# Optimization experiments

Measured on AMD Instinct MI355X. Metric: run time of the kernel, lower is better.

The kernel has to match this reference:

```python
import jax, jax.numpy as jnp
import numpy as np

N, DIN = 8192, 768
DH1, DO1 = 64, 64
DH2, DO2 = 32, 64


def setup_inputs() -> dict:
    key = jax.random.key(0)
    ks = jax.random.split(key, 12)
    s = lambda *sh: 0.02
    inp = {
        "X": jax.random.normal(ks[0], (N, DIN), jnp.float32),
        "A": jax.random.randint(ks[1], (N, N), 0, 2, jnp.int32),
        # GAT layer 1: W (din->dh), a (2dh), W2 (dh->dout) + bias
        "W1": jax.random.normal(ks[2], (DIN, DH1), jnp.float32) * 0.02,
        "a1": jax.random.normal(ks[3], (2 * DH1,), jnp.float32) * 0.02,
        "W21": jax.random.normal(ks[4], (DH1, DO1), jnp.float32) * 0.02,
        "b21": jnp.zeros((DO1,), jnp.float32),
        # GAT layer 2
        "Wg2": jax.random.normal(ks[5], (DO1, DH2), jnp.float32) * 0.02,
        "a2": jax.random.normal(ks[6], (2 * DH2,), jnp.float32) * 0.02,
        "W22": jax.random.normal(ks[7], (DH2, DO2), jnp.float32) * 0.02,
        "b22": jnp.zeros((DO2,), jnp.float32),
        # MLP head: 64 -> 64 -> 2
        "M1": jax.random.normal(ks[8], (DO2, 64), jnp.float32) * 0.02,
        "bm1": jnp.zeros((64,), jnp.float32),
        "M2": jax.random.normal(ks[9], (64, 2), jnp.float32) * 0.02,
        "bm2": jnp.zeros((2,), jnp.float32),
    }
    return inp


def _tiny_gat(X, A, W, a, W2, b2):
    # H = X @ W; e_ij = a . [H_i, H_j] = H_i@a_src + H_j@a_dst (same math,
    # no N x N x 2dh intermediate)
    H = X @ W                      # [N, dh]
    dh = W.shape[1]
    e = (H @ a[:dh])[:, None] + (H @ a[dh:])[None, :]   # [N, N]
    e = jnp.where(A == 0, jnp.float32(-1e9), e)
    alpha = jax.nn.softmax(e, axis=1)                   # softmax over neighbors j
    Z = alpha @ H                                       # [N, dh]
    return jax.nn.elu(Z @ W2 + b2)


def reference(X, A, W1, a1, W21, b21, Wg2, a2, W22, b22, M1, bm1, M2, bm2):
    Z = _tiny_gat(X, A, W1, a1, W21, b21)    # [N, 64]
    Z = _tiny_gat(Z, A, Wg2, a2, W22, b22)   # [N, 64]
    g = Z.mean(axis=0)                       # [64]
    h = jax.nn.relu(g @ M1 + bm1)
    return h @ M2 + bm2                      # [2]
```

## Files before the change

kernel.cpp:

```cpp
#include <hip/hip_runtime.h>


#define NN 8192

typedef __attribute__((ext_vector_type(8))) short s16x8;
typedef __attribute__((ext_vector_type(4))) float f32x4;
union V16 { uint4 u; s16x8 s; };

static constexpr size_t OFF_WBITS = 0;
static constexpr size_t OFF_GT1H  = (size_t)8 << 20;
static constexpr size_t OFF_GT1L  = (size_t)9 << 20;
static constexpr size_t OFF_U1    = (size_t)10 << 20;
static constexpr size_t OFF_DEN1  = ((size_t)10 << 20) + 32 * 1024;
static constexpr size_t OFF_GT2H  = ((size_t)10 << 20) + 128 * 1024;
static constexpr size_t OFF_GT2L  = ((size_t)10 << 20) + 896 * 1024;
static constexpr size_t OFF_GPART = ((size_t)11 << 20) + 768 * 1024;
static constexpr size_t OFF_NUMP  = (size_t)12 << 20;

__device__ __forceinline__ float elu_f(float x) {
    return x > 0.f ? x : expm1f(x);
}
__device__ __forceinline__ unsigned int bf16_rne(float x) {
    unsigned int u = __float_as_uint(x);
    return (u + 0x7FFFu + ((u >> 16) & 1u)) >> 16;
}
__device__ __forceinline__ unsigned int split_pack(float g) {
    unsigned int hi = bf16_rne(g);
    float fhi = __uint_as_float(hi << 16);
    unsigned int lo = bf16_rne(g - fhi);
    return (hi << 16) | lo;
}

__global__ __launch_bounds__(512) void k_xw1(const float* __restrict__ X,
                                             const float* __restrict__ W1,
                                             const float* __restrict__ a1,
                                             unsigned int* __restrict__ Gt1h,
                                             unsigned int* __restrict__ Gt1l,
                                             float* __restrict__ u1) {
    __shared__ float Xt[32][65];
    __shared__ float red[32][17];
    __shared__ float us[32];
    __shared__ unsigned int Gsh[64][33];
    const int tid = threadIdx.x;
    const int row = tid & 31, cg = tid >> 5;
    const int row0 = blockIdx.x * 32;
    float acc[4];
#pragma unroll
    for (int i = 0; i < 4; ++i) acc[i] = 0.f;
    const float4* X4 = (const float4*)X;
    for (int k0 = 0; k0 < 768; k0 += 64) {
        __syncthreads();
        {
            int r = tid >> 4, q = tid & 15;
            float4 v = X4[(size_t)(row0 + r) * 192 + (k0 >> 2) + q];
            Xt[r][q * 4 + 0] = v.x; Xt[r][q * 4 + 1] = v.y;
            Xt[r][q * 4 + 2] = v.z; Xt[r][q * 4 + 3] = v.w;
        }
        __syncthreads();
        const float4* W4 = (const float4*)(W1 + (size_t)k0 * 64);
        for (int kk = 0; kk < 64; ++kk) {
            float x = Xt[row][kk];
            float4 w = W4[kk * 16 + cg];
            acc[0] += x * w.x; acc[1] += x * w.y;
            acc[2] += x * w.z; acc[3] += x * w.w;
        }
    }
    float p = 0.f;
#pragma unroll
    for (int i = 0; i < 4; ++i) p += acc[i] * a1[64 + cg * 4 + i];
    red[row][cg] = p;
    __syncthreads();
    if (tid < 32) {
        float d = 0.f;
#pragma unroll
        for (int g = 0; g < 16; ++g) d += red[tid][g];
        float uv = expf(d);
        u1[row0 + tid] = uv;
        us[tid] = uv;
    }
    __syncthreads();
    float uv = us[row];
#pragma unroll
    for (int i = 0; i < 4; ++i)
        Gsh[cg * 4 + i][row] = split_pack(acc[i] * uv);
    __syncthreads();
    if (tid < 256) {
        const int mt = tid >> 6, lane = tid & 63;
        const int feat = mt * 16 + (lane & 15), quad = lane >> 4;
        uint4 hv, lv;
        unsigned int g0, g1;
#define PACK_Q(Q, FX)                                            \
        g0 = Gsh[feat][quad * 8 + 2 * Q];                        \
        g1 = Gsh[feat][quad * 8 + 2 * Q + 1];                    \
        hv.FX = (g0 >> 16) | (g1 & 0xFFFF0000u);                 \
        lv.FX = (g0 & 0xFFFFu) | (g1 << 16);
        PACK_Q(0, x) PACK_Q(1, y) PACK_Q(2, z) PACK_Q(3, w)
#undef PACK_Q
        size_t base = ((size_t)(mt * 256 + blockIdx.x) * 64 + lane) * 4;
        *(uint4*)(Gt1h + base) = hv;
        *(uint4*)(Gt1l + base) = lv;
    }
}

__global__ __launch_bounds__(256) void k_pack(const int* __restrict__ A,
                                              const float* __restrict__ u1,
                                              unsigned int* __restrict__ Wb32,
                                              float* __restrict__ den1) {
    __shared__ unsigned short msh[8][512];
    const int tid = threadIdx.x, wv = tid >> 6, lane = tid & 63;
    const int row0 = blockIdx.x * 8;
    float dsum0 = 0.f, dsum1 = 0.f;
    const int r0 = row0 + wv * 2, r1 = r0 + 1;
    for (int c = 0; c < 8; ++c) {
        const int j = c * 1024 + lane * 16;
        const int4* A0 = (const int4*)(A + (size_t)r0 * NN + j);
        const int4* A1 = (const int4*)(A + (size_t)r1 * NN + j);
        const float4* U4 = (const float4*)(u1 + j);
        int4 a0 = A0[0], a1 = A0[1], a2 = A0[2], a3 = A0[3];
        int4 b0 = A1[0], b1 = A1[1], b2 = A1[2], b3 = A1[3];
        float4 u0 = U4[0], u4 = U4[1], u8 = U4[2], uc = U4[3];
        unsigned int m0 = 0, m1 = 0;
#define DO4(AV, BV, UV, SH)                                            \
        m0 |= ((AV.x != 0) << (SH)) | ((AV.y != 0) << (SH + 1)) |      \
              ((AV.z != 0) << (SH + 2)) | ((AV.w != 0) << (SH + 3));   \
        m1 |= ((BV.x != 0) << (SH)) | ((BV.y != 0) << (SH + 1)) |      \
              ((BV.z != 0) << (SH + 2)) | ((BV.w != 0) << (SH + 3));   \
        dsum0 += (AV.x != 0 ? UV.x : 0.f) + (AV.y != 0 ? UV.y : 0.f) + \
                 (AV.z != 0 ? UV.z : 0.f) + (AV.w != 0 ? UV.w : 0.f);  \
        dsum1 += (BV.x != 0 ? UV.x : 0.f) + (BV.y != 0 ? UV.y : 0.f) + \
                 (BV.z != 0 ? UV.z : 0.f) + (BV.w != 0 ? UV.w : 0.f);
        DO4(a0, b0, u0, 0) DO4(a1, b1, u4, 4) DO4(a2, b2, u8, 8) DO4(a3, b3, uc, 12)
#undef DO4
        msh[wv * 2 + 0][c * 64 + lane] = (unsigned short)m0;
        msh[wv * 2 + 1][c * 64 + lane] = (unsigned short)m1;
    }
#pragma unroll
    for (int off = 32; off; off >>= 1) {
        dsum0 += __shfl_down(dsum0, off);
        dsum1 += __shfl_down(dsum1, off);
    }
    if (lane == 0) { den1[r0] = dsum0; den1[r1] = dsum1; }
    __syncthreads();
    {
        const int r = tid >> 5, i = tid & 31;
        const uint4* src = (const uint4*)&msh[r][0];
        uint4* dst = (uint4*)(Wb32 + (size_t)(row0 + r) * 256);
        dst[i] = src[i];
        dst[i + 32] = src[i + 32];
    }
}

__device__ __forceinline__ void build_lut(uint4* lut, int tid) {
    unsigned int b = (unsigned int)(tid & 255);
    uint4 e;
    e.x = ((b & 1u)   ? 0x3F80u : 0u) | ((b & 2u)   ? 0x3F800000u : 0u);
    e.y = ((b & 4u)   ? 0x3F80u : 0u) | ((b & 8u)   ? 0x3F800000u : 0u);
    e.z = ((b & 16u)  ? 0x3F80u : 0u) | ((b & 32u)  ? 0x3F800000u : 0u);
    e.w = ((b & 64u)  ? 0x3F80u : 0u) | ((b & 128u) ? 0x3F800000u : 0u);
    if (tid < 256) lut[tid] = e;
}

__global__ __launch_bounds__(256) void k_attn1(const unsigned int* __restrict__ Wb32,
                                               const unsigned int* __restrict__ Gt1h,
                                               const unsigned int* __restrict__ Gt1l,
                                               float* __restrict__ num1p) {
    __shared__ uint4 lut[256];
    __shared__ unsigned int bw[64 * 20];
    const int tid = threadIdx.x, wv = tid >> 6, lane = tid & 63;
    const int node0 = blockIdx.x * 64;
    const int kt0 = blockIdx.y * 16;
    build_lut(lut, tid);
    {
        const int r = tid >> 2, part = tid & 3;
        const uint4* src = (const uint4*)(Wb32 + (size_t)(node0 + r) * 256 + kt0 + part * 4);
        *(uint4*)&bw[r * 20 + part * 4] = src[0];
    }
    __syncthreads();
    const int n = lane & 15, quad = lane >> 4;
    const int brow = (wv * 16 + n) * 20;
    f32x4 acc[4];
#pragma unroll
    for (int mt = 0; mt < 4; ++mt) acc[mt] = (f32x4){0.f, 0.f, 0.f, 0.f};
#pragma unroll 2
    for (int ks = 0; ks < 16; ++ks) {
        unsigned int bits = bw[brow + ks];
        unsigned int byt = (bits >> (quad * 8)) & 0xFFu;
        V16 bf; bf.u = lut[byt];
#pragma unroll
        for (int mt = 0; mt < 4; ++mt) {
            size_t base = ((size_t)(mt * 256 + kt0 + ks) * 64 + lane) * 4;
            V16 ah, al;
            ah.u = *(const uint4*)(Gt1h + base);
            al.u = *(const uint4*)(Gt1l + base);
            acc[mt] = __builtin_amdgcn_mfma_f32_16x16x32_bf16(ah.s, bf.s, acc[mt], 0, 0, 0);
            acc[mt] = __builtin_amdgcn_mfma_f32_16x16x32_bf16(al.s, bf.s, acc[mt], 0, 0, 0);
        }
    }
    const int node = node0 + wv * 16 + n;
    const int s = blockIdx.y;
#pragma unroll
    for (int mt = 0; mt < 4; ++mt)
        *(f32x4*)&num1p[((size_t)s * NN + node) * 64 + mt * 16 + quad * 4] = acc[mt];
}

__global__ __launch_bounds__(512) void k_ep1(const float* __restrict__ num1p,
                                             const float* __restrict__ den1,
                                             const float* __restrict__ W21,
                                             const float* __restrict__ b21,
                                             const float* __restrict__ Wg2,
                                             const float* __restrict__ a2,
                                             unsigned int* __restrict__ Gt2h,
                                             unsigned int* __restrict__ Gt2l) {
    __shared__ float w21sh[64 * 64];
    __shared__ float wg2sh[64 * 32];
    __shared__ float zsh[8][64];
    __shared__ float osh[8][64];
    __shared__ unsigned int g2sh[32][33];
    __shared__ unsigned int u2sh[32];
    const int tid = threadIdx.x, wv = tid >> 6, lane = tid & 63;
    const int node0 = blockIdx.x * 32;
    {
        const float4* s4 = (const float4*)W21;
        float4* d4 = (float4*)w21sh;
        d4[tid] = s4[tid];
        d4[tid + 512] = s4[tid + 512];
        ((float4*)wg2sh)[tid] = ((const float4*)Wg2)[tid];
    }
    const float bb = b21[lane];
    const int l32 = lane & 31;
    const float a2v = (lane < 32) ? a2[32 + l32] : 0.f;
    __syncthreads();
    for (int it = 0; it < 4; ++it) {
        const int node = node0 + wv * 4 + it;
        float sacc = 0.f;
#pragma unroll
        for (int sp = 0; sp < 16; ++sp)
            sacc += num1p[((size_t)sp * NN + node) * 64 + lane];
        zsh[wv][lane] = sacc / den1[node];
        __builtin_amdgcn_wave_barrier();
        float o0 = 0.f, o1 = 0.f, o2 = 0.f, o3 = 0.f;
        for (int c = 0; c < 64; c += 4) {
            o0 += zsh[wv][c + 0] * w21sh[(c + 0) * 64 + lane];
            o1 += zsh[wv][c + 1] * w21sh[(c + 1) * 64 + lane];
            o2 += zsh[wv][c + 2] * w21sh[(c + 2) * 64 + lane];
            o3 += zsh[wv][c + 3] * w21sh[(c + 3) * 64 + lane];
        }
        float o = elu_f(bb + ((o0 + o1) + (o2 + o3)));
        osh[wv][lane] = o;
        __builtin_amdgcn_wave_barrier();
        float h0 = 0.f, h1 = 0.f;
        for (int c = 0; c < 64; c += 2) {
            h0 += osh[wv][c + 0] * wg2sh[(c + 0) * 32 + l32];
            h1 += osh[wv][c + 1] * wg2sh[(c + 1) * 32 + l32];
        }
        float hval = h0 + h1;
        float pp = hval * a2v;
#pragma unroll
        for (int off = 32; off; off >>= 1) pp += __shfl_down(pp, off);
        float d2 = __shfl(pp, 0);
        float uu = expf(d2);
        const int nodeloc = wv * 4 + it;
        if (lane == 0) u2sh[nodeloc] = split_pack(uu);
        if (lane < 32) g2sh[l32][nodeloc] = split_pack(uu * hval);
    }
    __syncthreads();
    if (tid < 192) {
        const int mt = tid >> 6, lane2 = tid & 63;
        const int ml = lane2 & 15, quad = lane2 >> 4;
        uint4 hv, lv;
        unsigned int g0, g1;
#define PACK_Q(Q, F)                                                   \
        {                                                              \
            int j0 = quad * 8 + 2 * Q;                                 \
            if (mt < 2) { g0 = g2sh[mt * 16 + ml][j0];                 \
                          g1 = g2sh[mt * 16 + ml][j0 + 1]; }           \
            else if (ml == 0) { g0 = u2sh[j0]; g1 = u2sh[j0 + 1]; }    \
            else { g0 = 0; g1 = 0; }                                   \
            hv.F = (g0 >> 16) | (g1 & 0xFFFF0000u);                    \
            lv.F = (g0 & 0xFFFFu) | (g1 << 16);                        \
        }
        PACK_Q(0, x) PACK_Q(1, y) PACK_Q(2, z) PACK_Q(3, w)
#undef PACK_Q
        size_t base = ((size_t)(mt * 256 + blockIdx.x) * 64 + lane2) * 4;
        *(uint4*)(Gt2h + base) = hv;
        *(uint4*)(Gt2l + base) = lv;
    }
}

__global__ __launch_bounds__(256) void k_attn2(const unsigned int* __restrict__ Wb32,
                                               const unsigned int* __restrict__ Gt2h,
                                               const unsigned int* __restrict__ Gt2l,
                                               float* __restrict__ num2p) {
    __shared__ uint4 lut[256];
    __shared__ unsigned int bw[64 * 20];
    const int tid = threadIdx.x, wv = tid >> 6, lane = tid & 63;
    const int node0 = blockIdx.x * 64;
    const int kt0 = blockIdx.y * 16;
    build_lut(lut, tid);
    {
        const int r = tid >> 2, part = tid & 3;
        const uint4* src = (const uint4*)(Wb32 + (size_t)(node0 + r) * 256 + kt0 + part * 4);
        *(uint4*)&bw[r * 20 + part * 4] = src[0];
    }
    __syncthreads();
    const int n = lane & 15, quad = lane >> 4;
    const int brow = (wv * 16 + n) * 20;
    f32x4 acc[3];
#pragma unroll
    for (int mt = 0; mt < 3; ++mt) acc[mt] = (f32x4){0.f, 0.f, 0.f, 0.f};
#pragma unroll 2
    for (int ks = 0; ks < 16; ++ks) {
        unsigned int bits = bw[brow + ks];
        unsigned int byt = (bits >> (quad * 8)) & 0xFFu;
        V16 bf; bf.u = lut[byt];
#pragma unroll
        for (int mt = 0; mt < 3; ++mt) {
            size_t base = ((size_t)(mt * 256 + kt0 + ks) * 64 + lane) * 4;
            V16 ah, al;
            ah.u = *(const uint4*)(Gt2h + base);
            al.u = *(const uint4*)(Gt2l + base);
            acc[mt] = __builtin_amdgcn_mfma_f32_16x16x32_bf16(ah.s, bf.s, acc[mt], 0, 0, 0);
            acc[mt] = __builtin_amdgcn_mfma_f32_16x16x32_bf16(al.s, bf.s, acc[mt], 0, 0, 0);
        }
    }
    const int node = node0 + wv * 16 + n;
    const int s = blockIdx.y;
#pragma unroll
    for (int mt = 0; mt < 3; ++mt)
        *(f32x4*)&num2p[((size_t)s * NN + node) * 48 + mt * 16 + quad * 4] = acc[mt];
}

__global__ __launch_bounds__(512) void k_ep2(const float* __restrict__ num2p,
                                             const float* __restrict__ W22,
                                             const float* __restrict__ b22,
                                             float* __restrict__ gpart) {
    __shared__ float w22sh[32 * 64];
    __shared__ float zsh[8][32];
    __shared__ float gsh[8][64];
    const int tid = threadIdx.x, wv = tid >> 6, lane = tid & 63;
    ((float4*)w22sh)[tid] = ((const float4*)W22)[tid];
    const float bb = b22[lane];
    __syncthreads();
    const int row = blockIdx.x * 8 + wv;
    float val = 0.f;
    if (lane < 33) {
#pragma unroll
        for (int sp = 0; sp < 16; ++sp)
            val += num2p[((size_t)sp * NN + row) * 48 + lane];
    }
    float den = __shfl(val, 32);
    if (lane < 32) zsh[wv][lane] = val / den;
    __builtin_amdgcn_wave_barrier();
    float o0 = 0.f, o1 = 0.f;
    for (int c = 0; c < 32; c += 2) {
        o0 += zsh[wv][c + 0] * w22sh[(c + 0) * 64 + lane];
        o1 += zsh[wv][c + 1] * w22sh[(c + 1) * 64 + lane];
    }
    gsh[wv][lane] = elu_f(bb + o0 + o1);
    __syncthreads();
    if (tid < 64) {
        float s = 0.f;
#pragma unroll
        for (int w = 0; w < 8; ++w) s += gsh[w][tid];
        gpart[(size_t)blockIdx.x * 64 + tid] = s;
    }
}

__global__ __launch_bounds__(256) void k_head(const float* __restrict__ gpart,
                                              const float* __restrict__ M1,
                                              const float* __restrict__ bm1,
                                              const float* __restrict__ M2,
                                              const float* __restrict__ bm2,
                                              float* __restrict__ outp) {
    __shared__ float part[4][64];
    __shared__ float gsh[64];
    __shared__ float hsh[64];
    const int tid = threadIdx.x, col = tid & 63, p = tid >> 6;
    float s = 0.f;
    for (int b = p * 256; b < p * 256 + 256; ++b)
        s += gpart[(size_t)b * 64 + col];
    part[p][col] = s;
    __syncthreads();
    if (tid < 64)
        gsh[tid] = (part[0][tid] + part[1][tid] + part[2][tid] + part[3][tid])
                   * (1.0f / 8192.0f);
    __syncthreads();
    if (tid < 64) {
        float h = bm1[tid];
        for (int c = 0; c < 64; ++c) h += gsh[c] * M1[c * 64 + tid];
        hsh[tid] = h > 0.f ? h : 0.f;
    }
    __syncthreads();
    if (tid < 2) {
        float o = bm2[tid];
        for (int j = 0; j < 64; ++j) o += hsh[j] * M2[j * 2 + tid];
        outp[tid] = o;
    }
}

extern "C" void kernel_launch(void* const* d_in, const int* in_sizes, int n_in,
                              void* d_out, int out_size, void* d_ws, size_t ws_size,
                              hipStream_t stream) {
    const float* X   = (const float*)d_in[0];
    const int*   A   = (const int*)  d_in[1];
    const float* W1  = (const float*)d_in[2];
    const float* a1  = (const float*)d_in[3];
    const float* W21 = (const float*)d_in[4];
    const float* b21 = (const float*)d_in[5];
    const float* Wg2 = (const float*)d_in[6];
    const float* a2  = (const float*)d_in[7];
    const float* W22 = (const float*)d_in[8];
    const float* b22 = (const float*)d_in[9];
    const float* M1  = (const float*)d_in[10];
    const float* bm1 = (const float*)d_in[11];
    const float* M2  = (const float*)d_in[12];
    const float* bm2 = (const float*)d_in[13];
    float* out = (float*)d_out;

    char* ws = (char*)d_ws;
    unsigned int* Wbits = (unsigned int*)(ws + OFF_WBITS);
    unsigned int* Gt1h  = (unsigned int*)(ws + OFF_GT1H);
    unsigned int* Gt1l  = (unsigned int*)(ws + OFF_GT1L);
    unsigned int* Gt2h  = (unsigned int*)(ws + OFF_GT2H);
    unsigned int* Gt2l  = (unsigned int*)(ws + OFF_GT2L);
    float* u1    = (float*)(ws + OFF_U1);
    float* den1  = (float*)(ws + OFF_DEN1);
    float* gpart = (float*)(ws + OFF_GPART);
    float* nump  = (float*)(ws + OFF_NUMP);

    k_xw1  <<<256, 512, 0, stream>>>(X, W1, a1, Gt1h, Gt1l, u1);
    k_pack <<<1024, 256, 0, stream>>>(A, u1, Wbits, den1);
    k_attn1<<<dim3(128, 16), 256, 0, stream>>>(Wbits, Gt1h, Gt1l, nump);
    k_ep1  <<<256, 512, 0, stream>>>(nump, den1, W21, b21, Wg2, a2, Gt2h, Gt2l);
    k_attn2<<<dim3(128, 16), 256, 0, stream>>>(Wbits, Gt2h, Gt2l, nump);
    k_ep2  <<<1024, 512, 0, stream>>>(nump, W22, b22, gpart);
    k_head <<<1, 256, 0, stream>>>(gpart, M1, bm1, M2, bm2, out);
}
```

Before: 591.1 us.

## Move X@W1 to split-bf16 MFMA and restructure attention waves by feature tile

The scalar FP32 X@W1 GEMM is replaced by a split-K MFMA kernel. X is split three ways and W1 two ways into bf16 pieces to keep near-fp32 accuracy, W1 is pre-packed by a setup kernel, and a combine kernel reduces the partials, computes u1 and packs Gt1. The attention kernels now give each wave one feature tile and loop over four node tiles. This loads each G fragment once per wave instead of per feature tile, and the shared-memory LUT is replaced by arithmetic bit-to-bf16 expansion. It adds extra launches and a partial-sum buffer, and in attn2 one wave idles.

```diff
diff --git a/kernel.cpp b/kernel.cpp
--- a/kernel.cpp
+++ b/kernel.cpp
@@ -16,6 +16,9 @@
 static constexpr size_t OFF_GT2L  = ((size_t)10 << 20) + 896 * 1024;
 static constexpr size_t OFF_GPART = ((size_t)11 << 20) + 768 * 1024;
 static constexpr size_t OFF_NUMP  = (size_t)12 << 20;
+static constexpr size_t OFF_WTAH  = (size_t)44 << 20;
+static constexpr size_t OFF_WTAL  = ((size_t)44 << 20) + 128 * 1024;
+static constexpr size_t OFF_DP    = (size_t)45 << 20;
 
 __device__ __forceinline__ float elu_f(float x) {
     return x > 0.f ? x : expm1f(x);
@@ -30,70 +33,144 @@
     unsigned int lo = bf16_rne(g - fhi);
     return (hi << 16) | lo;
 }
-
-__global__ __launch_bounds__(512) void k_xw1(const float* __restrict__ X,
-                                             const float* __restrict__ W1,
-                                             const float* __restrict__ a1,
-                                             unsigned int* __restrict__ Gt1h,
-                                             unsigned int* __restrict__ Gt1l,
-                                             float* __restrict__ u1) {
-    __shared__ float Xt[32][65];
-    __shared__ float red[32][17];
+__device__ __forceinline__ void split3(float f, unsigned int& h, unsigned int& m,
+                                       unsigned int& l) {
+    h = bf16_rne(f);
+    float fh = __uint_as_float(h << 16);
+    float r1 = f - fh;
+    m = bf16_rne(r1);
+    float fm = __uint_as_float(m << 16);
+    l = bf16_rne(r1 - fm);
+}
+__device__ __forceinline__ unsigned int bits2bf(unsigned int b2) {
+    return (b2 & 1u) * 0x3F80u + (b2 & 2u) * 0x1FC00000u;
+}
+
+__global__ __launch_bounds__(256) void k_wsetup(const float* __restrict__ W1,
+                                                unsigned int* __restrict__ WtAh,
+                                                unsigned int* __restrict__ WtAl) {
+    const int t = blockIdx.x * 256 + threadIdx.x;
+    const int tile = t >> 6, lane = t & 63;
+    const int mt = tile / 24, kt = tile % 24;
+    const int feat = mt * 16 + (lane & 15), quad = lane >> 4;
+    uint4 hv, lv;
+    unsigned int h0, l0, h1, l1;
+#define WQ(Q, F)                                                        \
+    {                                                                   \
+        int k0 = kt * 32 + quad * 8 + 2 * Q;                            \
+        float w0 = W1[(size_t)k0 * 64 + feat];                          \
+        float w1 = W1[(size_t)(k0 + 1) * 64 + feat];                    \
+        h0 = bf16_rne(w0); l0 = bf16_rne(w0 - __uint_as_float(h0 << 16));\
+        h1 = bf16_rne(w1); l1 = bf16_rne(w1 - __uint_as_float(h1 << 16));\
+        hv.F = h0 | (h1 << 16);                                         \
+        lv.F = l0 | (l1 << 16);                                         \
+    }
+    WQ(0, x) WQ(1, y) WQ(2, z) WQ(3, w)
+#undef WQ
+    size_t base = (size_t)((mt * 24 + kt) * 64 + lane) * 4;
+    *(uint4*)(WtAh + base) = hv;
+    *(uint4*)(WtAl + base) = lv;
+}
+
+__global__ __launch_bounds__(256) void k_xw1m(const float* __restrict__ X,
+                                              const unsigned int* __restrict__ WtAh,
+                                              const unsigned int* __restrict__ WtAl,
+                                              float* __restrict__ Dp) {
+    const int tid = threadIdx.x, wv = tid >> 6, lane = tid & 63;
+    const int n = lane & 15, quad = lane >> 4;
+    const int node = blockIdx.x * 64 + wv * 16 + n;
+    const int ntg = blockIdx.x * 4 + wv;
+    const int ks = blockIdx.y;
+    f32x4 acc[4];
+#pragma unroll
+    for (int mt = 0; mt < 4; ++mt) acc[mt] = (f32x4){0.f, 0.f, 0.f, 0.f};
+    const float4* X4 = (const float4*)X;
+    for (int kk = 0; kk < 6; ++kk) {
+        const int kt = ks * 6 + kk;
+        float4 x01 = X4[(size_t)node * 192 + kt * 8 + quad * 2];
+        float4 x23 = X4[(size_t)node * 192 + kt * 8 + quad * 2 + 1];
+        float xf[8] = {x01.x, x01.y, x01.z, x01.w, x23.x, x23.y, x23.z, x23.w};
+        V16 bh, bm, bl;
+        unsigned int* bhp = (unsigned int*)&bh.u;
+        unsigned int* bmp = (unsigned int*)&bm.u;
+        unsigned int* blp = (unsigned int*)&bl.u;
+#pragma unroll
+        for (int q = 0; q < 4; ++q) {
+            unsigned int h0, m0, l0, h1, m1, l1;
+            split3(xf[2 * q], h0, m0, l0);
+            split3(xf[2 * q + 1], h1, m1, l1);
+            bhp[q] = h0 | (h1 << 16);
+            bmp[q] = m0 | (m1 << 16);
+            blp[q] = l0 | (l1 << 16);
+        }
+#pragma unroll
+        for (int mt = 0; mt < 4; ++mt) {
+            size_t base = (size_t)((mt * 24 + kt) * 64 + lane) * 4;
+            V16 awh, awl;
+            awh.u = *(const uint4*)(WtAh + base);
+            awl.u = *(const uint4*)(WtAl + base);
+            acc[mt] = __builtin_amdgcn_mfma_f32_16x16x32_bf16(awh.s, bh.s, acc[mt], 0, 0, 0);
+            acc[mt] = __builtin_amdgcn_mfma_f32_16x16x32_bf16(awh.s, bm.s, acc[mt], 0, 0, 0);
+            acc[mt] = __builtin_amdgcn_mfma_f32_16x16x32_bf16(awh.s, bl.s, acc[mt], 0, 0, 0);
+            acc[mt] = __builtin_amdgcn_mfma_f32_16x16x32_bf16(awl.s, bh.s, acc[mt], 0, 0, 0);
+            acc[mt] = __builtin_amdgcn_mfma_f32_16x16x32_bf16(awl.s, bm.s, acc[mt], 0, 0, 0);
+        }
+    }
+#pragma unroll
+    for (int mt = 0; mt < 4; ++mt)
+        *(f32x4*)&Dp[(size_t)(((ks * 4 + mt) * 512 + ntg) * 64 + lane) * 4] = acc[mt];
+}
+
+__global__ __launch_bounds__(256) void k_xcomb(const float* __restrict__ Dp,
+                                               const float* __restrict__ a1,
+                                               unsigned int* __restrict__ Gt1h,
+                                               unsigned int* __restrict__ Gt1l,
+                                               float* __restrict__ u1) {
+    __shared__ float Hsh[64][33];
     __shared__ float us[32];
-    __shared__ unsigned int Gsh[64][33];
     const int tid = threadIdx.x;
-    const int row = tid & 31, cg = tid >> 5;
-    const int row0 = blockIdx.x * 32;
-    float acc[4];
-#pragma unroll
-    for (int i = 0; i < 4; ++i) acc[i] = 0.f;
-    const float4* X4 = (const float4*)X;
-    for (int k0 = 0; k0 < 768; k0 += 64) {
-        __syncthreads();
-        {
-            int r = tid >> 4, q = tid & 15;
-            float4 v = X4[(size_t)(row0 + r) * 192 + (k0 >> 2) + q];
-            Xt[r][q * 4 + 0] = v.x; Xt[r][q * 4 + 1] = v.y;
-            Xt[r][q * 4 + 2] = v.z; Xt[r][q * 4 + 3] = v.w;
-        }
-        __syncthreads();
-        const float4* W4 = (const float4*)(W1 + (size_t)k0 * 64);
-        for (int kk = 0; kk < 64; ++kk) {
-            float x = Xt[row][kk];
-            float4 w = W4[kk * 16 + cg];
-            acc[0] += x * w.x; acc[1] += x * w.y;
-            acc[2] += x * w.z; acc[3] += x * w.w;
-        }
-    }
-    float p = 0.f;
-#pragma unroll
-    for (int i = 0; i < 4; ++i) p += acc[i] * a1[64 + cg * 4 + i];
-    red[row][cg] = p;
-    __syncthreads();
-    if (tid < 32) {
-        float d = 0.f;
-#pragma unroll
-        for (int g = 0; g < 16; ++g) d += red[tid][g];
-        float uv = expf(d);
-        u1[row0 + tid] = uv;
-        us[tid] = uv;
-    }
-    __syncthreads();
-    float uv = us[row];
-#pragma unroll
-    for (int i = 0; i < 4; ++i)
-        Gsh[cg * 4 + i][row] = split_pack(acc[i] * uv);
-    __syncthreads();
-    if (tid < 256) {
+    if (tid < 128) {
+        const int ntl = tid >> 6, lane = tid & 63;
+        const int n = lane & 15, quad = lane >> 4;
+        const int ntg = blockIdx.x * 2 + ntl;
+        float dpart = 0.f;
+#pragma unroll
+        for (int mt = 0; mt < 4; ++mt) {
+            float v[4] = {0.f, 0.f, 0.f, 0.f};
+#pragma unroll
+            for (int ksp = 0; ksp < 4; ++ksp) {
+                const float* p = &Dp[(size_t)(((ksp * 4 + mt) * 512 + ntg) * 64 + lane) * 4];
+                v[0] += p[0]; v[1] += p[1]; v[2] += p[2]; v[3] += p[3];
+            }
+#pragma unroll
+            for (int r = 0; r < 4; ++r) {
+                int feat = mt * 16 + quad * 4 + r;
+                Hsh[feat][ntl * 16 + n] = v[r];
+                dpart += v[r] * a1[64 + feat];
+            }
+        }
+        dpart += __shfl_xor(dpart, 16);
+        dpart += __shfl_xor(dpart, 32);
+        float uu = expf(dpart);
+        if (lane < 16) {
+            us[ntl * 16 + lane] = uu;
+            u1[blockIdx.x * 32 + ntl * 16 + lane] = uu;
+        }
+    }
+    __syncthreads();
+    {
         const int mt = tid >> 6, lane = tid & 63;
         const int feat = mt * 16 + (lane & 15), quad = lane >> 4;
         uint4 hv, lv;
         unsigned int g0, g1;
-#define PACK_Q(Q, FX)                                            \
-        g0 = Gsh[feat][quad * 8 + 2 * Q];                        \
-        g1 = Gsh[feat][quad * 8 + 2 * Q + 1];                    \
-        hv.FX = (g0 >> 16) | (g1 & 0xFFFF0000u);                 \
-        lv.FX = (g0 & 0xFFFFu) | (g1 << 16);
+#define PACK_Q(Q, FX)                                                   \
+        {                                                               \
+            int j0 = quad * 8 + 2 * Q;                                  \
+            g0 = split_pack(us[j0] * Hsh[feat][j0]);                    \
+            g1 = split_pack(us[j0 + 1] * Hsh[feat][j0 + 1]);            \
+            hv.FX = (g0 >> 16) | (g1 & 0xFFFF0000u);                    \
+            lv.FX = (g0 & 0xFFFFu) | (g1 << 16);                        \
+        }
         PACK_Q(0, x) PACK_Q(1, y) PACK_Q(2, z) PACK_Q(3, w)
 #undef PACK_Q
         size_t base = ((size_t)(mt * 256 + blockIdx.x) * 64 + lane) * 4;
@@ -150,26 +227,14 @@
     }
 }
 
-__device__ __forceinline__ void build_lut(uint4* lut, int tid) {
-    unsigned int b = (unsigned int)(tid & 255);
-    uint4 e;
-    e.x = ((b & 1u)   ? 0x3F80u : 0u) | ((b & 2u)   ? 0x3F800000u : 0u);
-    e.y = ((b & 4u)   ? 0x3F80u : 0u) | ((b & 8u)   ? 0x3F800000u : 0u);
-    e.z = ((b & 16u)  ? 0x3F80u : 0u) | ((b & 32u)  ? 0x3F800000u : 0u);
-    e.w = ((b & 64u)  ? 0x3F80u : 0u) | ((b & 128u) ? 0x3F800000u : 0u);
-    if (tid < 256) lut[tid] = e;
-}
-
 __global__ __launch_bounds__(256) void k_attn1(const unsigned int* __restrict__ Wb32,
                                                const unsigned int* __restrict__ Gt1h,
                                                const unsigned int* __restrict__ Gt1l,
                                                float* __restrict__ num1p) {
-    __shared__ uint4 lut[256];
     __shared__ unsigned int bw[64 * 20];
     const int tid = threadIdx.x, wv = tid >> 6, lane = tid & 63;
     const int node0 = blockIdx.x * 64;
     const int kt0 = blockIdx.y * 16;
-    build_lut(lut, tid);
     {
         const int r = tid >> 2, part = tid & 3;
         const uint4* src = (const uint4*)(Wb32 + (size_t)(node0 + r) * 256 + kt0 + part * 4);
@@ -177,30 +242,32 @@
     }
     __syncthreads();
     const int n = lane & 15, quad = lane >> 4;
-    const int brow = (wv * 16 + n) * 20;
+    const int mt = wv;
     f32x4 acc[4];
 #pragma unroll
-    for (int mt = 0; mt < 4; ++mt) acc[mt] = (f32x4){0.f, 0.f, 0.f, 0.f};
-#pragma unroll 2
+    for (int nt = 0; nt < 4; ++nt) acc[nt] = (f32x4){0.f, 0.f, 0.f, 0.f};
+#pragma unroll 4
     for (int ks = 0; ks < 16; ++ks) {
-        unsigned int bits = bw[brow + ks];
-        unsigned int byt = (bits >> (quad * 8)) & 0xFFu;
-        V16 bf; bf.u = lut[byt];
-#pragma unroll
-        for (int mt = 0; mt < 4; ++mt) {
-            size_t base = ((size_t)(mt * 256 + kt0 + ks) * 64 + lane) * 4;
-            V16 ah, al;
-            ah.u = *(const uint4*)(Gt1h + base);
-            al.u = *(const uint4*)(Gt1l + base);
-            acc[mt] = __builtin_amdgcn_mfma_f32_16x16x32_bf16(ah.s, bf.s, acc[mt], 0, 0, 0);
-            acc[mt] = __builtin_amdgcn_mfma_f32_16x16x32_bf16(al.s, bf.s, acc[mt], 0, 0, 0);
-        }
-    }
-    const int node = node0 + wv * 16 + n;
+        size_t base = ((size_t)(mt * 256 + kt0 + ks) * 64 + lane) * 4;
+        V16 ah, al;
+        ah.u = *(const uint4*)(Gt1h + base);
+        al.u = *(const uint4*)(Gt1l + base);
+#pragma unroll
+        for (int nt = 0; nt < 4; ++nt) {
+            unsigned int by8 = (bw[(nt * 16 + n) * 20 + ks] >> (quad * 8)) & 0xFFu;
+            V16 bf;
+            bf.u = make_uint4(bits2bf(by8), bits2bf(by8 >> 2),
+                              bits2bf(by8 >> 4), bits2bf(by8 >> 6));
+            acc[nt] = __builtin_amdgcn_mfma_f32_16x16x32_bf16(ah.s, bf.s, acc[nt], 0, 0, 0);
+            acc[nt] = __builtin_amdgcn_mfma_f32_16x16x32_bf16(al.s, bf.s, acc[nt], 0, 0, 0);
+        }
+    }
     const int s = blockIdx.y;
 #pragma unroll
-    for (int mt = 0; mt < 4; ++mt)
-        *(f32x4*)&num1p[((size_t)s * NN + node) * 64 + mt * 16 + quad * 4] = acc[mt];
+    for (int nt = 0; nt < 4; ++nt) {
+        const int node = node0 + nt * 16 + n;
+        *(f32x4*)&num1p[((size_t)s * NN + node) * 64 + mt * 16 + quad * 4] = acc[nt];
+    }
 }
 
 __global__ __launch_bounds__(512) void k_ep1(const float* __restrict__ num1p,
@@ -291,43 +358,44 @@
                                                const unsigned int* __restrict__ Gt2h,
                                                const unsigned int* __restrict__ Gt2l,
                                                float* __restrict__ num2p) {
-    __shared__ uint4 lut[256];
     __shared__ unsigned int bw[64 * 20];
     const int tid = threadIdx.x, wv = tid >> 6, lane = tid & 63;
     const int node0 = blockIdx.x * 64;
     const int kt0 = blockIdx.y * 16;
-    build_lut(lut, tid);
     {
         const int r = tid >> 2, part = tid & 3;
         const uint4* src = (const uint4*)(Wb32 + (size_t)(node0 + r) * 256 + kt0 + part * 4);
         *(uint4*)&bw[r * 20 + part * 4] = src[0];
     }
     __syncthreads();
+    if (wv == 3) return;
     const int n = lane & 15, quad = lane >> 4;
-    const int brow = (wv * 16 + n) * 20;
-    f32x4 acc[3];
-#pragma unroll
-    for (int mt = 0; mt < 3; ++mt) acc[mt] = (f32x4){0.f, 0.f, 0.f, 0.f};
-#pragma unroll 2
+    const int mt = wv;
+    f32x4 acc[4];
+#pragma unroll
+    for (int nt = 0; nt < 4; ++nt) acc[nt] = (f32x4){0.f, 0.f, 0.f, 0.f};
+#pragma unroll 4
     for (int ks = 0; ks < 16; ++ks) {
-        unsigned int bits = bw[brow + ks];
-        unsigned int byt = (bits >> (quad * 8)) & 0xFFu;
-        V16 bf; bf.u = lut[byt];
-#pragma unroll
-        for (int mt = 0; mt < 3; ++mt) {
-            size_t base = ((size_t)(mt * 256 + kt0 + ks) * 64 + lane) * 4;
-            V16 ah, al;
-            ah.u = *(const uint4*)(Gt2h + base);
-            al.u = *(const uint4*)(Gt2l + base);
-            acc[mt] = __builtin_amdgcn_mfma_f32_16x16x32_bf16(ah.s, bf.s, acc[mt], 0, 0, 0);
-            acc[mt] = __builtin_amdgcn_mfma_f32_16x16x32_bf16(al.s, bf.s, acc[mt], 0, 0, 0);
-        }
-    }
-    const int node = node0 + wv * 16 + n;
+        size_t base = ((size_t)(mt * 256 + kt0 + ks) * 64 + lane) * 4;
+        V16 ah, al;
+        ah.u = *(const uint4*)(Gt2h + base);
+        al.u = *(const uint4*)(Gt2l + base);
+#pragma unroll
+        for (int nt = 0; nt < 4; ++nt) {
+            unsigned int by8 = (bw[(nt * 16 + n) * 20 + ks] >> (quad * 8)) & 0xFFu;
+            V16 bf;
+            bf.u = make_uint4(bits2bf(by8), bits2bf(by8 >> 2),
+                              bits2bf(by8 >> 4), bits2bf(by8 >> 6));
+            acc[nt] = __builtin_amdgcn_mfma_f32_16x16x32_bf16(ah.s, bf.s, acc[nt], 0, 0, 0);
+            acc[nt] = __builtin_amdgcn_mfma_f32_16x16x32_bf16(al.s, bf.s, acc[nt], 0, 0, 0);
+        }
+    }
     const int s = blockIdx.y;
 #pragma unroll
-    for (int mt = 0; mt < 3; ++mt)
-        *(f32x4*)&num2p[((size_t)s * NN + node) * 48 + mt * 16 + quad * 4] = acc[mt];
+    for (int nt = 0; nt < 4; ++nt) {
+        const int node = node0 + nt * 16 + n;
+        *(f32x4*)&num2p[((size_t)s * NN + node) * 48 + mt * 16 + quad * 4] = acc[nt];
+    }
 }
 
 __global__ __launch_bounds__(512) void k_ep2(const float* __restrict__ num2p,
@@ -423,12 +491,17 @@
     unsigned int* Gt1l  = (unsigned int*)(ws + OFF_GT1L);
     unsigned int* Gt2h  = (unsigned int*)(ws + OFF_GT2H);
     unsigned int* Gt2l  = (unsigned int*)(ws + OFF_GT2L);
+    unsigned int* WtAh  = (unsigned int*)(ws + OFF_WTAH);
+    unsigned int* WtAl  = (unsigned int*)(ws + OFF_WTAL);
+    float* Dp    = (float*)(ws + OFF_DP);
     float* u1    = (float*)(ws + OFF_U1);
     float* den1  = (float*)(ws + OFF_DEN1);
     float* gpart = (float*)(ws + OFF_GPART);
     float* nump  = (float*)(ws + OFF_NUMP);
 
-    k_xw1  <<<256, 512, 0, stream>>>(X, W1, a1, Gt1h, Gt1l, u1);
+    k_wsetup<<<24, 256, 0, stream>>>(W1, WtAh, WtAl);
+    k_xw1m <<<dim3(128, 4), 256, 0, stream>>>(X, WtAh, WtAl, Dp);
+    k_xcomb<<<256, 256, 0, stream>>>(Dp, a1, Gt1h, Gt1l, u1);
     k_pack <<<1024, 256, 0, stream>>>(A, u1, Wbits, den1);
     k_attn1<<<dim3(128, 16), 256, 0, stream>>>(Wbits, Gt1h, Gt1l, nump);
     k_ep1  <<<256, 512, 0, stream>>>(nump, den1, W21, b21, Wg2, a2, Gt2h, Gt2l);
```

New measurement: 512.4 us. 1.15x faster.
